# Optimization experiments

Hardware: AMD Instinct MI355X
Metric: run time of the kernel (lower is better)

Reference implementation:

```python
import jax, jax.numpy as jnp
import numpy as np

B, OBS, TASK = 65536, 512, 128
D, M, N = 64, 32, 4  # embedding dim, module width, modules per layer


def setup_inputs() -> dict:
    key = jax.random.key(0)
    ks = jax.random.split(key, 16)

    def w(k, shape):
        fan_in = shape[-2]
        return jax.random.normal(k, shape, jnp.float32) * np.float32(np.sqrt(2.0 / fan_in))

    z = lambda *s: jnp.zeros(s, jnp.float32)
    return dict(
        obs=jax.random.normal(ks[0], (B, OBS), jnp.float32),
        task=jax.random.normal(ks[1], (B, TASK), jnp.float32),
        Ws1=w(ks[2], (OBS, D)), bs1=z(D),
        Ws2=w(ks[3], (D, D)), bs2=z(D),
        Wt=w(ks[4], (TASK, D)), bt=z(D),
        Wa0=w(ks[5], (D, N * N)), ba0=z(N * N),
        Wa1=w(ks[6], (D, N * N)), ba1=z(N * N),
        Wc0=w(ks[7], (N * N, D)), bc0=z(D),
        Wc1=w(ks[8], (2 * N * N, D)), bc1=z(D),
        We0=w(ks[9], (N, D, M)), be0=z(N, M),
        We1=w(ks[10], (N, M, M)), be1=z(N, M),
        We2=w(ks[11], (N, M, M)), be2=z(N, M),
    )


def reference(obs, task, Ws1, bs1, Ws2, bs2, Wt, bt, Wa0, ba0, Wa1, ba1,
              Wc0, bc0, Wc1, bc1, We0, be0, We1, be1, We2, be2):
    relu = jax.nn.relu
    # base encoders
    s = relu(relu(obs @ Ws1 + bs1) @ Ws2 + bs2)          # [B, D]
    t = relu(task @ Wt + bt)                              # [B, D]
    r0 = s * t                                            # first routing inputs [B, D]
    prev = jnp.broadcast_to(s[None], (N,) + s.shape)      # [N, B, D] (state emb fed to all layer-0 modules)

    # routing layer 0 -> 1
    a0 = jax.nn.softmax((r0 @ Wa0 + ba0).reshape(-1, N, N), axis=-1)   # [B, N_next, N_prev]
    m = relu(jnp.einsum('nbi,nio->nbo', prev, We0) + be0[:, None, :])  # [N, B, M] expert outputs
    prev = jnp.einsum('bij,jbd->ibd', a0, m)                           # [N, B, M] attention-combined
    r = relu((a0.reshape(-1, N * N) @ Wc0 + bc0) * r0)                 # updated routing inputs

    # routing layer 1 -> 2
    a1 = jax.nn.softmax((r @ Wa1 + ba1).reshape(-1, N, N), axis=-1)
    m = relu(jnp.einsum('nbi,nio->nbo', prev, We1) + be1[:, None, :])
    prev = jnp.einsum('bij,jbd->ibd', a1, m)
    attn_cat = jnp.concatenate([a0.reshape(-1, N * N), a1.reshape(-1, N * N)], axis=-1)
    r = relu((attn_cat @ Wc1 + bc1) * r0)  # computed as in original (unused afterward)

    # final module layer, plain sum over modules
    m = relu(jnp.einsum('nbi,nio->nbo', prev, We2) + be2[:, None, :])  # [N, B, M]
    return relu(m.sum(axis=0))                                          # [B, M]
```

## Files before the change

### kernel.cpp

```cpp
#include <hip/hip_runtime.h>
#include <hip/hip_bf16.h>


using f32x4 = __attribute__((ext_vector_type(4))) float;
using h16x4 = __attribute__((ext_vector_type(4))) _Float16;
using u32x4 = __attribute__((ext_vector_type(4))) unsigned int;
using u32x2 = __attribute__((ext_vector_type(2))) unsigned int;

#define MFMA16(a, b, c) __builtin_amdgcn_mfma_f32_16x16x16f16((a), (b), (c), 0, 0, 0)

__device__ __forceinline__ short h_bits(float f) {
  _Float16 h = (_Float16)f;
  return __builtin_bit_cast(short, h);
}

__device__ __forceinline__ void dma16(const float* g, char* l) {
  __builtin_amdgcn_global_load_lds(
      (const __attribute__((address_space(1))) unsigned int*)g,
      (__attribute__((address_space(3))) unsigned int*)l, 16, 0, 0);
}

__global__ void sm_convert_v7(
    const float* __restrict__ Ws1, const float* __restrict__ Ws2, const float* __restrict__ Wt,
    const float* __restrict__ Wa0, const float* __restrict__ Wa1, const float* __restrict__ Wc0,
    const float* __restrict__ We0, const float* __restrict__ We1, const float* __restrict__ We2,
    const float* __restrict__ bs1, const float* __restrict__ bs2, const float* __restrict__ bt,
    const float* __restrict__ ba0, const float* __restrict__ ba1, const float* __restrict__ bc0,
    const float* __restrict__ be0, const float* __restrict__ be1, const float* __restrict__ be2,
    short* __restrict__ wsh, float* __restrict__ biasf) {
  int d = blockIdx.x * 256 + threadIdx.x;
  if (d < 64512) {
    float v;
    if (d < 32768) {
      int kk = d & 3, nt = (d >> 2) & 3, p = (d >> 4) & 15, q = (d >> 8) & 3, cc = d >> 10;
      int k = cc * 16 + q * 4 + kk, o = nt * 16 + p;
      v = Ws1[k * 64 + o];
    }
    else if (d < 36864) { int r = d - 32768, o = r >> 6, k = r & 63;   v = Ws2[k * 64 + o]; }
    else if (d < 45056) {
      int r = d - 36864;
      int kk = r & 3, nt = (r >> 2) & 3, p = (r >> 4) & 15, q = (r >> 8) & 3, cc = r >> 10;
      int k = cc * 16 + q * 4 + kk, o = nt * 16 + p;
      v = Wt[k * 64 + o];
    }
    else if (d < 46080) { int r = d - 45056, o = r >> 6, k = r & 63;   v = Wa0[k * 16 + o]; }
    else if (d < 47104) { int r = d - 46080, o = r >> 6, k = r & 63;   v = Wa1[k * 16 + o]; }
    else if (d < 48128) { int r = d - 47104, o = r >> 4, k = r & 15;   v = Wc0[k * 64 + o]; }
    else if (d < 56320) { int r = d - 48128, n = r >> 11, o = (r >> 6) & 31, i = r & 63; v = We0[n * 2048 + i * 32 + o]; }
    else if (d < 60416) { int r = d - 56320, n = r >> 10, o = (r >> 5) & 31, i = r & 31; v = We1[n * 1024 + i * 32 + o]; }
    else                { int r = d - 60416, n = r >> 10, o = (r >> 5) & 31, i = r & 31; v = We2[n * 1024 + i * 32 + o]; }
    wsh[d] = h_bits(v);
  } else if (d < 65184) {
    int r = d - 64512;
    float v;
    if      (r < 64)  v = bs1[r];
    else if (r < 128) v = bs2[r - 64];
    else if (r < 192) v = bt[r - 128];
    else if (r < 208) v = ba0[r - 192];
    else if (r < 224) v = ba1[r - 208];
    else if (r < 288) v = bc0[r - 224];
    else if (r < 416) v = be0[r - 288];
    else if (r < 544) v = be1[r - 416];
    else              v = be2[r - 544];
    biasf[r] = v;
  }
}

__global__ __launch_bounds__(256) void sm_fused_v7(
    const float* __restrict__ obs, const float* __restrict__ task,
    const short* __restrict__ wsh, const float* __restrict__ biasf,
    float* __restrict__ out) {
  const int tid  = threadIdx.x;
  const int wave = tid >> 6;
  const int lane = tid & 63;
  const int q    = lane >> 4;
  const int p    = lane & 15;
  const int lrow = wave * 16;
  const int wgrow  = blockIdx.x * 64;
  const int rowblk = wgrow + lrow;

  __shared__ __align__(16) char lds[28672];
  char* x_lds = lds;
  char* a_lds = lds + 9216;
  char* ring  = lds + 12288;
  char* p_lds = lds;

  const short* Bp1  = wsh;
  const short* Ws2T = wsh + 32768;
  const short* WtP  = wsh + 36864;
  const short* Wa0T = wsh + 45056;
  const short* Wa1T = wsh + 46080;
  const short* Wc0T = wsh + 47104;
  const short* We0T = wsh + 48128;
  const short* We1T = wsh + 56320;
  const short* We2T = wsh + 60416;
  const float* bs1 = biasf;        const float* bs2 = biasf + 64;
  const float* bt  = biasf + 128;  const float* ba0 = biasf + 192;
  const float* ba1 = biasf + 208;  const float* bc0 = biasf + 224;
  const float* be0 = biasf + 288;  const float* be1 = biasf + 416;
  const float* be2 = biasf + 544;

  const f32x4 z4 = {0.f, 0.f, 0.f, 0.f};

  auto stx  = [&](int row, int col, float v) { *(short*)(x_lds + row * 144 + col * 2) = h_bits(v); };
  auto ldx4 = [&](int row, int k0) -> h16x4 { return *(const h16x4*)(x_lds + row * 144 + k0 * 2); };
  auto ldb  = [&](const short* W, int off) -> h16x4 { return *(const h16x4*)(W + off); };
  auto cvtA = [&](const u32x4& u) -> h16x4 {
    float4 v = __builtin_bit_cast(float4, u);
    h16x4 a;
    a[0] = (_Float16)v.x; a[1] = (_Float16)v.y;
    a[2] = (_Float16)v.z; a[3] = (_Float16)v.w;
    return a;
  };
  auto lo2 = [&](const u32x4& u) -> h16x4 { return __builtin_bit_cast(h16x4, (u32x2){u[0], u[1]}); };
  auto hi2 = [&](const u32x4& u) -> h16x4 { return __builtin_bit_cast(h16x4, (u32x2){u[2], u[3]}); };

  auto stage = [&](const float* base, int rowlen, int k0, int buf) {
#pragma unroll
    for (int j = 0; j < 2; ++j) {
      int f = j * 256 + wave * 64 + lane;
      int row = f >> 3;
      int cl = (f & 7) ^ (row & 7);
      const float* g = base + (size_t)(wgrow + row) * rowlen + k0 + cl * 4;
      dma16(g, ring + buf * 8192 + (j * 256 + wave * 64) * 16);
    }
  };
  auto lda = [&](int buf, int kb2) -> u32x4 {
    return *(const u32x4*)(ring + buf * 8192 + (lrow + p) * 128 +
                           (((kb2 * 4 + q) ^ (p & 7)) * 16));
  };

  f32x4 accX[4] = {z4, z4, z4, z4};
  {
    stage(obs, 512, 0, 0);
    for (int c = 0; c < 16; ++c) {
      if (c + 1 < 16) {
        stage(obs, 512, (c + 1) * 32, (c + 1) & 1);
        asm volatile("s_waitcnt vmcnt(2)" ::: "memory");
      } else {
        asm volatile("s_waitcnt vmcnt(0)" ::: "memory");
      }
      __syncthreads();
#pragma unroll
      for (int kb2 = 0; kb2 < 2; ++kb2) {
        const int cc = c * 2 + kb2;
        const short* bp = Bp1 + ((cc * 4 + q) * 16 + p) * 16;
        u32x4 B0 = *(const u32x4*)bp;
        u32x4 B1 = *(const u32x4*)(bp + 8);
        h16x4 a = cvtA(lda(c & 1, kb2));
        accX[0] = MFMA16(a, lo2(B0), accX[0]);
        accX[1] = MFMA16(a, hi2(B0), accX[1]);
        accX[2] = MFMA16(a, lo2(B1), accX[2]);
        accX[3] = MFMA16(a, hi2(B1), accX[3]);
      }
      __syncthreads();
    }
  }
#pragma unroll
  for (int nt = 0; nt < 4; ++nt) {
    float bias = bs1[nt * 16 + p];
#pragma unroll
    for (int r = 0; r < 4; ++r)
      stx(lrow + 4 * q + r, nt * 16 + p, fmaxf(accX[nt][r] + bias, 0.f));
  }

  stage(task, 128, 0, 0);

  f32x4 accS[4] = {z4, z4, z4, z4};
#pragma unroll
  for (int kb = 0; kb < 4; ++kb) {
    h16x4 a = ldx4(lrow + p, kb * 16 + q * 4);
#pragma unroll
    for (int nt = 0; nt < 4; ++nt)
      accS[nt] = MFMA16(a, ldb(Ws2T, (nt * 16 + p) * 64 + kb * 16 + q * 4), accS[nt]);
  }
  float sf[4][4];
#pragma unroll
  for (int nt = 0; nt < 4; ++nt) {
    float bias = bs2[nt * 16 + p];
#pragma unroll
    for (int r = 0; r < 4; ++r) sf[nt][r] = fmaxf(accS[nt][r] + bias, 0.f);
  }
#pragma unroll
  for (int nt = 0; nt < 4; ++nt)
#pragma unroll
    for (int r = 0; r < 4; ++r) stx(lrow + 4 * q + r, nt * 16 + p, sf[nt][r]);

  f32x4 accT[4] = {z4, z4, z4, z4};
  {
    for (int c = 0; c < 4; ++c) {
      if (c + 1 < 4) {
        stage(task, 128, (c + 1) * 32, (c + 1) & 1);
        asm volatile("s_waitcnt vmcnt(2)" ::: "memory");
      } else {
        asm volatile("s_waitcnt vmcnt(0)" ::: "memory");
      }
      __syncthreads();
#pragma unroll
      for (int kb2 = 0; kb2 < 2; ++kb2) {
        const int cc = c * 2 + kb2;
        const short* bp = WtP + ((cc * 4 + q) * 16 + p) * 16;
        u32x4 B0 = *(const u32x4*)bp;
        u32x4 B1 = *(const u32x4*)(bp + 8);
        h16x4 a = cvtA(lda(c & 1, kb2));
        accT[0] = MFMA16(a, lo2(B0), accT[0]);
        accT[1] = MFMA16(a, hi2(B0), accT[1]);
        accT[2] = MFMA16(a, lo2(B1), accT[2]);
        accT[3] = MFMA16(a, hi2(B1), accT[3]);
      }
      __syncthreads();
    }
  }
  float r0f[4][4];
#pragma unroll
  for (int nt = 0; nt < 4; ++nt) {
    float bias = bt[nt * 16 + p];
#pragma unroll
    for (int r = 0; r < 4; ++r)
      r0f[nt][r] = sf[nt][r] * fmaxf(accT[nt][r] + bias, 0.f);
  }

  float mfr[4][2][4];
#pragma unroll
  for (int n = 0; n < 4; ++n) {
    f32x4 acc[2] = {z4, z4};
#pragma unroll
    for (int kb = 0; kb < 4; ++kb) {
      h16x4 a = ldx4(lrow + p, kb * 16 + q * 4);
#pragma unroll
      for (int nt = 0; nt < 2; ++nt)
        acc[nt] = MFMA16(a, ldb(We0T, (n * 32 + nt * 16 + p) * 64 + kb * 16 + q * 4), acc[nt]);
    }
#pragma unroll
    for (int nt = 0; nt < 2; ++nt) {
      float bias = be0[n * 32 + nt * 16 + p];
#pragma unroll
      for (int r = 0; r < 4; ++r) mfr[n][nt][r] = fmaxf(acc[nt][r] + bias, 0.f);
    }
  }

#pragma unroll
  for (int nt = 0; nt < 4; ++nt)
#pragma unroll
    for (int r = 0; r < 4; ++r) stx(lrow + 4 * q + r, nt * 16 + p, r0f[nt][r]);

  f32x4 accA = z4;
#pragma unroll
  for (int kb = 0; kb < 4; ++kb)
    accA = MFMA16(ldx4(lrow + p, kb * 16 + q * 4), ldb(Wa0T, p * 64 + kb * 16 + q * 4), accA);
  float a0v[4];
  {
    float bias = ba0[p];
#pragma unroll
    for (int r = 0; r < 4; ++r) {
      float v = accA[r] + bias;
      float mx = fmaxf(v, __shfl_xor(v, 1));
      mx = fmaxf(mx, __shfl_xor(mx, 2));
      float e = __expf(v - mx);
      float ssum = e + __shfl_xor(e, 1);
      ssum += __shfl_xor(ssum, 2);
      a0v[r] = e / ssum;
    }
  }
#pragma unroll
  for (int r = 0; r < 4; ++r)
    *(short*)(a_lds + (lrow + 4 * q + r) * 48 + p * 2) = h_bits(a0v[r]);

  float pv[4][2][4];
#pragma unroll
  for (int i = 0; i < 4; ++i)
#pragma unroll
    for (int nt = 0; nt < 2; ++nt)
#pragma unroll
      for (int r = 0; r < 4; ++r) pv[i][nt][r] = 0.f;
  const int sbase = lane & 48;
#pragma unroll
  for (int r = 0; r < 4; ++r) {
#pragma unroll
    for (int c = 0; c < 16; ++c) {
      float av = __shfl(a0v[r], sbase | c);
      pv[c >> 2][0][r] += av * mfr[c & 3][0][r];
      pv[c >> 2][1][r] += av * mfr[c & 3][1][r];
    }
  }

  f32x4 accC[4] = {z4, z4, z4, z4};
  {
    h16x4 a = *(const h16x4*)(a_lds + (lrow + p) * 48 + q * 8);
#pragma unroll
    for (int nt = 0; nt < 4; ++nt)
      accC[nt] = MFMA16(a, ldb(Wc0T, (nt * 16 + p) * 16 + q * 4), accC[nt]);
  }
  float rf[4][4];
#pragma unroll
  for (int nt = 0; nt < 4; ++nt) {
    float bias = bc0[nt * 16 + p];
#pragma unroll
    for (int r = 0; r < 4; ++r)
      rf[nt][r] = fmaxf((accC[nt][r] + bias) * r0f[nt][r], 0.f);
  }
#pragma unroll
  for (int nt = 0; nt < 4; ++nt)
#pragma unroll
    for (int r = 0; r < 4; ++r) stx(lrow + 4 * q + r, nt * 16 + p, rf[nt][r]);

  f32x4 accA1 = z4;
#pragma unroll
  for (int kb = 0; kb < 4; ++kb)
    accA1 = MFMA16(ldx4(lrow + p, kb * 16 + q * 4), ldb(Wa1T, p * 64 + kb * 16 + q * 4), accA1);
  float a1v[4];
  {
    float bias = ba1[p];
#pragma unroll
    for (int r = 0; r < 4; ++r) {
      float v = accA1[r] + bias;
      float mx = fmaxf(v, __shfl_xor(v, 1));
      mx = fmaxf(mx, __shfl_xor(mx, 2));
      float e = __expf(v - mx);
      float ssum = e + __shfl_xor(e, 1);
      ssum += __shfl_xor(ssum, 2);
      a1v[r] = e / ssum;
    }
  }

  __syncthreads();

#pragma unroll
  for (int i = 0; i < 4; ++i)
#pragma unroll
    for (int nt = 0; nt < 2; ++nt)
#pragma unroll
      for (int r = 0; r < 4; ++r)
        *(short*)(p_lds + (i * 64 + lrow + 4 * q + r) * 80 + (nt * 16 + p) * 2) = h_bits(pv[i][nt][r]);

  float m1f[4][2][4];
#pragma unroll
  for (int n = 0; n < 4; ++n) {
    f32x4 acc[2] = {z4, z4};
#pragma unroll
    for (int kb = 0; kb < 2; ++kb) {
      h16x4 a = *(const h16x4*)(p_lds + (n * 64 + lrow + p) * 80 + kb * 32 + q * 8);
#pragma unroll
      for (int nt = 0; nt < 2; ++nt)
        acc[nt] = MFMA16(a, ldb(We1T, (n * 32 + nt * 16 + p) * 32 + kb * 16 + q * 4), acc[nt]);
    }
#pragma unroll
    for (int nt = 0; nt < 2; ++nt) {
      float bias = be1[n * 32 + nt * 16 + p];
#pragma unroll
      for (int r = 0; r < 4; ++r) m1f[n][nt][r] = fmaxf(acc[nt][r] + bias, 0.f);
    }
  }

#pragma unroll
  for (int i = 0; i < 4; ++i)
#pragma unroll
    for (int nt = 0; nt < 2; ++nt)
#pragma unroll
      for (int r = 0; r < 4; ++r) pv[i][nt][r] = 0.f;
#pragma unroll
  for (int r = 0; r < 4; ++r) {
#pragma unroll
    for (int c = 0; c < 16; ++c) {
      float av = __shfl(a1v[r], sbase | c);
      pv[c >> 2][0][r] += av * m1f[c & 3][0][r];
      pv[c >> 2][1][r] += av * m1f[c & 3][1][r];
    }
  }

#pragma unroll
  for (int i = 0; i < 4; ++i)
#pragma unroll
    for (int nt = 0; nt < 2; ++nt)
#pragma unroll
      for (int r = 0; r < 4; ++r)
        *(short*)(p_lds + (i * 64 + lrow + 4 * q + r) * 80 + (nt * 16 + p) * 2) = h_bits(pv[i][nt][r]);

  float of[2][4] = {{0.f, 0.f, 0.f, 0.f}, {0.f, 0.f, 0.f, 0.f}};
#pragma unroll
  for (int n = 0; n < 4; ++n) {
    f32x4 acc[2] = {z4, z4};
#pragma unroll
    for (int kb = 0; kb < 2; ++kb) {
      h16x4 a = *(const h16x4*)(p_lds + (n * 64 + lrow + p) * 80 + kb * 32 + q * 8);
#pragma unroll
      for (int nt = 0; nt < 2; ++nt)
        acc[nt] = MFMA16(a, ldb(We2T, (n * 32 + nt * 16 + p) * 32 + kb * 16 + q * 4), acc[nt]);
    }
#pragma unroll
    for (int nt = 0; nt < 2; ++nt) {
      float bias = be2[n * 32 + nt * 16 + p];
#pragma unroll
      for (int r = 0; r < 4; ++r) of[nt][r] += fmaxf(acc[nt][r] + bias, 0.f);
    }
  }
#pragma unroll
  for (int nt = 0; nt < 2; ++nt)
#pragma unroll
    for (int r = 0; r < 4; ++r) {
      int grow = rowblk + 4 * q + r;
      out[(size_t)grow * 32 + nt * 16 + p] = of[nt][r];
    }
}

extern "C" void kernel_launch(void* const* d_in, const int* in_sizes, int n_in,
                              void* d_out, int out_size, void* d_ws, size_t ws_size,
                              hipStream_t stream) {
  (void)in_sizes; (void)n_in; (void)out_size; (void)ws_size;
  const float* obs  = (const float*)d_in[0];
  const float* task = (const float*)d_in[1];
  const float* Ws1 = (const float*)d_in[2];  const float* bs1 = (const float*)d_in[3];
  const float* Ws2 = (const float*)d_in[4];  const float* bs2 = (const float*)d_in[5];
  const float* Wt  = (const float*)d_in[6];  const float* bt  = (const float*)d_in[7];
  const float* Wa0 = (const float*)d_in[8];  const float* ba0 = (const float*)d_in[9];
  const float* Wa1 = (const float*)d_in[10]; const float* ba1 = (const float*)d_in[11];
  const float* Wc0 = (const float*)d_in[12]; const float* bc0 = (const float*)d_in[13];
  const float* We0 = (const float*)d_in[16]; const float* be0 = (const float*)d_in[17];
  const float* We1 = (const float*)d_in[18]; const float* be1 = (const float*)d_in[19];
  const float* We2 = (const float*)d_in[20]; const float* be2 = (const float*)d_in[21];

  short* wsh   = (short*)d_ws;
  float* biasf = (float*)((char*)d_ws + 129040);

  sm_convert_v7<<<dim3(255), dim3(256), 0, stream>>>(
      Ws1, Ws2, Wt, Wa0, Wa1, Wc0, We0, We1, We2,
      bs1, bs2, bt, ba0, ba1, bc0, be0, be1, be2,
      wsh, biasf);
  sm_fused_v7<<<dim3(1024), dim3(256), 0, stream>>>(
      obs, task, wsh, biasf, (float*)d_out);
}
```

Before: 79.67 us.

## Stage weight tiles into LDS via DMA alongside activations, single barrier per chunk

Ws1 and Wt weights are re-laid out so each 32-wide K chunk is contiguous, then DMA'd into an LDS ring next to the obs/task tiles instead of being read from global memory by every wave. The double-buffered loop now uses one wait-plus-barrier at the top of each iteration instead of two __syncthreads, and the first task stage is issued earlier so it overlaps the Ws1 epilogue. The x_lds row pitch shrinks from 144 to 136 bytes. Together these aim to cut global weight traffic and barrier stalls. The cost is a larger LDS footprint, which may lower occupancy, and a full vmcnt(0) wait each iteration.

```diff
diff --git a/kernel.cpp b/kernel.cpp
--- a/kernel.cpp
+++ b/kernel.cpp
@@ -14,13 +14,13 @@
   return __builtin_bit_cast(short, h);
 }
 
-__device__ __forceinline__ void dma16(const float* g, char* l) {
+__device__ __forceinline__ void dma16(const void* g, char* l) {
   __builtin_amdgcn_global_load_lds(
       (const __attribute__((address_space(1))) unsigned int*)g,
       (__attribute__((address_space(3))) unsigned int*)l, 16, 0, 0);
 }
 
-__global__ void sm_convert_v7(
+__global__ void sm_convert_v9(
     const float* __restrict__ Ws1, const float* __restrict__ Ws2, const float* __restrict__ Wt,
     const float* __restrict__ Wa0, const float* __restrict__ Wa1, const float* __restrict__ Wc0,
     const float* __restrict__ We0, const float* __restrict__ We1, const float* __restrict__ We2,
@@ -32,15 +32,29 @@
   if (d < 64512) {
     float v;
     if (d < 32768) {
-      int kk = d & 3, nt = (d >> 2) & 3, p = (d >> 4) & 15, q = (d >> 8) & 3, cc = d >> 10;
-      int k = cc * 16 + q * 4 + kk, o = nt * 16 + p;
+      int kk   = d & 3;
+      int ntip = (d >> 2) & 1;
+      int p    = (d >> 3) & 15;
+      int q    = (d >> 7) & 3;
+      int pair = (d >> 9) & 1;
+      int kb2  = (d >> 10) & 1;
+      int c    = d >> 11;
+      int k = c * 32 + kb2 * 16 + q * 4 + kk;
+      int o = pair * 32 + ntip * 16 + p;
       v = Ws1[k * 64 + o];
     }
     else if (d < 36864) { int r = d - 32768, o = r >> 6, k = r & 63;   v = Ws2[k * 64 + o]; }
     else if (d < 45056) {
       int r = d - 36864;
-      int kk = r & 3, nt = (r >> 2) & 3, p = (r >> 4) & 15, q = (r >> 8) & 3, cc = r >> 10;
-      int k = cc * 16 + q * 4 + kk, o = nt * 16 + p;
+      int kk   = r & 3;
+      int ntip = (r >> 2) & 1;
+      int p    = (r >> 3) & 15;
+      int q    = (r >> 7) & 3;
+      int pair = (r >> 9) & 1;
+      int kb2  = (r >> 10) & 1;
+      int c    = r >> 11;
+      int k = c * 32 + kb2 * 16 + q * 4 + kk;
+      int o = pair * 32 + ntip * 16 + p;
       v = Wt[k * 64 + o];
     }
     else if (d < 46080) { int r = d - 45056, o = r >> 6, k = r & 63;   v = Wa0[k * 16 + o]; }
@@ -66,7 +80,7 @@
   }
 }
 
-__global__ __launch_bounds__(256) void sm_fused_v7(
+__global__ __launch_bounds__(256) void sm_fused_v9(
     const float* __restrict__ obs, const float* __restrict__ task,
     const short* __restrict__ wsh, const float* __restrict__ biasf,
     float* __restrict__ out) {
@@ -79,10 +93,10 @@
   const int wgrow  = blockIdx.x * 64;
   const int rowblk = wgrow + lrow;
 
-  __shared__ __align__(16) char lds[28672];
+  __shared__ __align__(16) char lds[36352];
   char* x_lds = lds;
-  char* a_lds = lds + 9216;
-  char* ring  = lds + 12288;
+  char* a_lds = lds + 8704;
+  char* ring  = lds + 11776;
   char* p_lds = lds;
 
   const short* Bp1  = wsh;
@@ -102,8 +116,8 @@
 
   const f32x4 z4 = {0.f, 0.f, 0.f, 0.f};
 
-  auto stx  = [&](int row, int col, float v) { *(short*)(x_lds + row * 144 + col * 2) = h_bits(v); };
-  auto ldx4 = [&](int row, int k0) -> h16x4 { return *(const h16x4*)(x_lds + row * 144 + k0 * 2); };
+  auto stx  = [&](int row, int col, float v) { *(short*)(x_lds + row * 136 + col * 2) = h_bits(v); };
+  auto ldx4 = [&](int row, int k0) -> h16x4 { return *(const h16x4*)(x_lds + row * 136 + k0 * 2); };
   auto ldb  = [&](const short* W, int off) -> h16x4 { return *(const h16x4*)(W + off); };
   auto cvtA = [&](const u32x4& u) -> h16x4 {
     float4 v = __builtin_bit_cast(float4, u);
@@ -115,47 +129,56 @@
   auto lo2 = [&](const u32x4& u) -> h16x4 { return __builtin_bit_cast(h16x4, (u32x2){u[0], u[1]}); };
   auto hi2 = [&](const u32x4& u) -> h16x4 { return __builtin_bit_cast(h16x4, (u32x2){u[2], u[3]}); };
 
-  auto stage = [&](const float* base, int rowlen, int k0, int buf) {
+  auto stageA = [&](const float* base, int rowlen, int k0, int buf) {
 #pragma unroll
     for (int j = 0; j < 2; ++j) {
       int f = j * 256 + wave * 64 + lane;
       int row = f >> 3;
       int cl = (f & 7) ^ (row & 7);
-      const float* g = base + (size_t)(wgrow + row) * rowlen + k0 + cl * 4;
-      dma16(g, ring + buf * 8192 + (j * 256 + wave * 64) * 16);
+      dma16(base + (size_t)(wgrow + row) * rowlen + k0 + cl * 4,
+            ring + buf * 12288 + j * 4096 + wave * 1024);
     }
   };
-  auto lda = [&](int buf, int kb2) -> u32x4 {
-    return *(const u32x4*)(ring + buf * 8192 + (lrow + p) * 128 +
+  auto stageB = [&](const short* bsrc, int c, int buf) {
+    dma16((const char*)bsrc + c * 4096 + (wave * 64 + lane) * 16,
+          ring + buf * 12288 + 8192 + wave * 1024);
+  };
+  auto lda_ = [&](int buf, int kb2) -> u32x4 {
+    return *(const u32x4*)(ring + buf * 12288 + (lrow + p) * 128 +
                            (((kb2 * 4 + q) ^ (p & 7)) * 16));
   };
+  auto ldbs = [&](int buf, int kb2, int pair) -> u32x4 {
+    return *(const u32x4*)(ring + buf * 12288 + 8192 + kb2 * 2048 + pair * 1024 + lane * 16);
+  };
 
   f32x4 accX[4] = {z4, z4, z4, z4};
   {
-    stage(obs, 512, 0, 0);
+    stageA(obs, 512, 0, 0); stageB(Bp1, 0, 0);
     for (int c = 0; c < 16; ++c) {
+      asm volatile("s_waitcnt vmcnt(0)" ::: "memory");
+      __builtin_amdgcn_s_barrier();
+      __builtin_amdgcn_sched_barrier(0);
       if (c + 1 < 16) {
-        stage(obs, 512, (c + 1) * 32, (c + 1) & 1);
-        asm volatile("s_waitcnt vmcnt(2)" ::: "memory");
-      } else {
-        asm volatile("s_waitcnt vmcnt(0)" ::: "memory");
+        stageA(obs, 512, (c + 1) * 32, (c + 1) & 1);
+        stageB(Bp1, c + 1, (c + 1) & 1);
       }
-      __syncthreads();
+      __builtin_amdgcn_sched_barrier(0);
+      const int buf = c & 1;
 #pragma unroll
       for (int kb2 = 0; kb2 < 2; ++kb2) {
-        const int cc = c * 2 + kb2;
-        const short* bp = Bp1 + ((cc * 4 + q) * 16 + p) * 16;
-        u32x4 B0 = *(const u32x4*)bp;
-        u32x4 B1 = *(const u32x4*)(bp + 8);
-        h16x4 a = cvtA(lda(c & 1, kb2));
+        h16x4 a = cvtA(lda_(buf, kb2));
+        u32x4 B0 = ldbs(buf, kb2, 0);
+        u32x4 B1 = ldbs(buf, kb2, 1);
         accX[0] = MFMA16(a, lo2(B0), accX[0]);
         accX[1] = MFMA16(a, hi2(B0), accX[1]);
         accX[2] = MFMA16(a, lo2(B1), accX[2]);
         accX[3] = MFMA16(a, hi2(B1), accX[3]);
       }
-      __syncthreads();
-    }
-  }
+    }
+  }
+
+  stageA(task, 128, 0, 0); stageB(WtP, 0, 0);
+
 #pragma unroll
   for (int nt = 0; nt < 4; ++nt) {
     float bias = bs1[nt * 16 + p];
@@ -163,8 +186,6 @@
     for (int r = 0; r < 4; ++r)
       stx(lrow + 4 * q + r, nt * 16 + p, fmaxf(accX[nt][r] + bias, 0.f));
   }
-
-  stage(task, 128, 0, 0);
 
   f32x4 accS[4] = {z4, z4, z4, z4};
 #pragma unroll
@@ -189,26 +210,25 @@
   f32x4 accT[4] = {z4, z4, z4, z4};
   {
     for (int c = 0; c < 4; ++c) {
+      asm volatile("s_waitcnt vmcnt(0)" ::: "memory");
+      __builtin_amdgcn_s_barrier();
+      __builtin_amdgcn_sched_barrier(0);
       if (c + 1 < 4) {
-        stage(task, 128, (c + 1) * 32, (c + 1) & 1);
-        asm volatile("s_waitcnt vmcnt(2)" ::: "memory");
-      } else {
-        asm volatile("s_waitcnt vmcnt(0)" ::: "memory");
+        stageA(task, 128, (c + 1) * 32, (c + 1) & 1);
+        stageB(WtP, c + 1, (c + 1) & 1);
       }
-      __syncthreads();
+      __builtin_amdgcn_sched_barrier(0);
+      const int buf = c & 1;
 #pragma unroll
       for (int kb2 = 0; kb2 < 2; ++kb2) {
-        const int cc = c * 2 + kb2;
-        const short* bp = WtP + ((cc * 4 + q) * 16 + p) * 16;
-        u32x4 B0 = *(const u32x4*)bp;
-        u32x4 B1 = *(const u32x4*)(bp + 8);
-        h16x4 a = cvtA(lda(c & 1, kb2));
+        h16x4 a = cvtA(lda_(buf, kb2));
+        u32x4 B0 = ldbs(buf, kb2, 0);
+        u32x4 B1 = ldbs(buf, kb2, 1);
         accT[0] = MFMA16(a, lo2(B0), accT[0]);
         accT[1] = MFMA16(a, hi2(B0), accT[1]);
         accT[2] = MFMA16(a, lo2(B1), accT[2]);
         accT[3] = MFMA16(a, hi2(B1), accT[3]);
       }
-      __syncthreads();
     }
   }
   float r0f[4][4];
@@ -422,10 +442,10 @@
   short* wsh   = (short*)d_ws;
   float* biasf = (float*)((char*)d_ws + 129040);
 
-  sm_convert_v7<<<dim3(255), dim3(256), 0, stream>>>(
+  sm_convert_v9<<<dim3(255), dim3(256), 0, stream>>>(
       Ws1, Ws2, Wt, Wa0, Wa1, Wc0, We0, We1, We2,
       bs1, bs2, bt, ba0, ba1, bc0, be0, be1, be2,
       wsh, biasf);
-  sm_fused_v7<<<dim3(1024), dim3(256), 0, stream>>>(
+  sm_fused_v9<<<dim3(1024), dim3(256), 0, stream>>>(
       obs, task, wsh, biasf, (float*)d_out);
 }
```

Measured after the change: 71.32 us. -10.5%, faster.
